# Optimization experiments

Hardware: AMD Instinct MI355X
Metric: run time of the kernel (lower is better)

Reference implementation:

```python
import jax, jax.numpy as jnp
import numpy as np

B, S, E, H = 2, 2048, 2048, 16
D = E // H  # head_dim = 128


def _rope_tables(seq_len, dim):
    # standard RoPE: theta_i = 10000^(-2i/dim), angles duplicated over pair halves
    inv_freq = 1.0 / (10000.0 ** (np.arange(0, dim, 2, dtype=np.float32) / dim))
    angles = np.arange(seq_len, dtype=np.float32)[:, None] * inv_freq[None, :]  # [S, D/2]
    angles = np.concatenate([angles, angles], axis=-1)  # [S, D]
    return jnp.asarray(np.cos(angles)), jnp.asarray(np.sin(angles))


def setup_inputs() -> dict:
    key = jax.random.key(0)
    ks = jax.random.split(key, 10)
    sc = 1.0 / np.sqrt(E)
    cos, sin = _rope_tables(S, D)
    mask = jnp.tril(jnp.ones((S, S), dtype=bool))[None, None]  # causal [1,1,S,S]
    return {
        "x_q": jax.random.normal(ks[0], (B, S, E), jnp.float32),
        "x_kv": jax.random.normal(ks[1], (B, S, E), jnp.float32),
        "cos": cos,
        "sin": sin,
        "wq": jax.random.normal(ks[2], (E, E), jnp.float32) * sc,
        "bq": jax.random.normal(ks[3], (E,), jnp.float32) * 0.01,
        "wk": jax.random.normal(ks[4], (E, E), jnp.float32) * sc,
        "bk": jax.random.normal(ks[5], (E,), jnp.float32) * 0.01,
        "wv": jax.random.normal(ks[6], (E, E), jnp.float32) * sc,
        "bv": jax.random.normal(ks[7], (E,), jnp.float32) * 0.01,
        "wo": jax.random.normal(ks[8], (E, E), jnp.float32) * sc,
        "bo": jax.random.normal(ks[9], (E,), jnp.float32) * 0.01,
        "mask": mask,
    }


def _apply_rope(x, cos, sin):
    # x: [B,H,S,D]; cos/sin: [S,D]. rotate-half convention.
    x1, x2 = jnp.split(x, 2, axis=-1)
    rot = jnp.concatenate([-x2, x1], axis=-1)
    return x * cos[None, None] + rot * sin[None, None]


def reference(x_q, x_kv, cos, sin, wq, bq, wk, bk, wv, bv, wo, bo, mask):
    b, sq, _ = x_q.shape
    skv = x_kv.shape[1]
    q = (x_q @ wq.T + bq).reshape(b, sq, H, D).transpose(0, 2, 1, 3)   # [B,H,Sq,D]
    k = (x_kv @ wk.T + bk).reshape(b, skv, H, D).transpose(0, 2, 1, 3)
    v = (x_kv @ wv.T + bv).reshape(b, skv, H, D).transpose(0, 2, 1, 3)
    q = _apply_rope(q, cos, sin)
    k = _apply_rope(k, cos, sin)
    scores = jnp.einsum("bhqd,bhkd->bhqk", q, k) / jnp.sqrt(jnp.float32(D))
    scores = jnp.where(mask, scores, jnp.float32(-1e9))
    w = jax.nn.softmax(scores, axis=-1)  # dropout p=0 -> identity
    out = jnp.einsum("bhqk,bhkd->bhqd", w, v)
    out = out.transpose(0, 2, 1, 3).reshape(b, sq, H * D)
    return out @ wo.T + bo
```

## Files before the change

kernel.cpp:

```cpp
#include <hip/hip_runtime.h>
#include <hip/hip_bf16.h>

#define Bb 2
#define Ss 2048
#define Ee 2048
#define Hh 16
#define Dd 128
#define Mrows (Bb*Ss)

typedef short short8 __attribute__((ext_vector_type(8)));
typedef float f32x4 __attribute__((ext_vector_type(4)));

__device__ __forceinline__ unsigned short bf_rne(float f) {
    unsigned u = __builtin_bit_cast(unsigned, f);
    u += 0x7fffu + ((u >> 16) & 1u);
    return (unsigned short)(u >> 16);
}
__device__ __forceinline__ float bf2f(unsigned short x) {
    unsigned u = ((unsigned)x) << 16;
    return __builtin_bit_cast(float, u);
}
__device__ __forceinline__ void load_lds16(const void* g, void* l) {
    __builtin_amdgcn_global_load_lds(
        (const __attribute__((address_space(1))) unsigned int*)g,
        (__attribute__((address_space(3))) unsigned int*)l, 16, 0, 0);
}

__global__ void cast_all_kernel(const float4* __restrict__ xq, const float4* __restrict__ xkv,
                                const float4* __restrict__ wq, const float4* __restrict__ wk,
                                const float4* __restrict__ wv, const float4* __restrict__ wo,
                                ushort4* __restrict__ out) {
    int i = blockIdx.x * 256 + threadIdx.x;
    const float4* src;
    int rel;
    if (i < 2097152)       { src = xq;  rel = i; }
    else if (i < 4194304)  { src = xkv; rel = i - 2097152; }
    else if (i < 5242880)  { src = wq;  rel = i - 4194304; }
    else if (i < 6291456)  { src = wk;  rel = i - 5242880; }
    else if (i < 7340032)  { src = wv;  rel = i - 6291456; }
    else                   { src = wo;  rel = i - 7340032; }
    float4 v = src[rel];
    ushort4 o;
    o.x = bf_rne(v.x); o.y = bf_rne(v.y); o.z = bf_rne(v.z); o.w = bf_rne(v.w);
    out[i] = o;
}

#define NTK 64

__device__ __forceinline__ void gemm_core_db(
    const short* __restrict__ A, const short* __restrict__ W,
    int m0, int n0, char* lds, f32x4 (&acc)[8][4], int tid)
{
    const int wid  = tid >> 6, lane = tid & 63;
    const int wr   = wid >> 1, wc   = wid & 1;
    const int quad = lane >> 4, l16 = lane & 15;
    const int lr   = lane >> 3, sl  = lane & 7;
    const int g    = sl ^ lr;
    const int grow = 2*(wid*8 + lr) + (g >> 2);
    const int kcol = (g & 3) * 8;
    const int cx16 = ((((l16 & 1) << 2) + quad) ^ ((l16 >> 1) & 7)) << 4;
    const int arow = (l16 >> 1) << 7;

    const short* Ap = A + (size_t)(m0 + grow) * Ee + kcol;
    const short* Wp = W + (size_t)(n0 + grow) * Ee + kcol;

    #pragma unroll
    for (int i = 0; i < 4; ++i)
        load_lds16(Ap + (size_t)i*64*Ee, lds + i*4096 + wid*1024);
    #pragma unroll
    for (int i = 0; i < 2; ++i)
        load_lds16(Wp + (size_t)i*64*Ee, lds + 16384 + i*4096 + wid*1024);
    Ap += 32; Wp += 32;
    asm volatile("s_waitcnt vmcnt(0)\n\ts_barrier" ::: "memory");

    for (int t = 0; t < NTK; ++t) {
        const int bo = (t & 1) ? 24576 : 0;
        if (t + 1 < NTK) {
            const int so = bo ^ 24576;
            #pragma unroll
            for (int i = 0; i < 4; ++i)
                load_lds16(Ap + (size_t)i*64*Ee, lds + so + i*4096 + wid*1024);
            #pragma unroll
            for (int i = 0; i < 2; ++i)
                load_lds16(Wp + (size_t)i*64*Ee, lds + so + 16384 + i*4096 + wid*1024);
            Ap += 32; Wp += 32;
        }
        const char* Ab2 = lds + bo + wr*8192 + arow + cx16;
        const char* Bb2 = lds + bo + 16384 + wc*4096 + arow + cx16;
        short8 bfr[4];
        #pragma unroll
        for (int j = 0; j < 4; ++j) bfr[j] = *(const short8*)(Bb2 + j*1024);
        __builtin_amdgcn_s_setprio(1);
        #pragma unroll
        for (int i = 0; i < 8; ++i) {
            short8 af = *(const short8*)(Ab2 + i*1024);
            #pragma unroll
            for (int j = 0; j < 4; ++j)
                acc[i][j] = __builtin_amdgcn_mfma_f32_16x16x32_bf16(af, bfr[j], acc[i][j], 0, 0, 0);
        }
        __builtin_amdgcn_s_setprio(0);
        asm volatile("s_waitcnt vmcnt(0)\n\ts_barrier" ::: "memory");
    }
}

#define BUFB 24576

__device__ __forceinline__ void gemm_core(
    const short* __restrict__ A, const short* __restrict__ W,
    int m0, int n0, char* lds, f32x4 (&acc)[8][4], int tid)
{
    const int wid  = tid >> 6, lane = tid & 63;
    const int wr   = wid >> 1, wc   = wid & 1;
    const int quad = lane >> 4, l16 = lane & 15;
    const int lr   = lane >> 3, sl  = lane & 7;
    const int g    = sl ^ lr;
    const int grow = 2*(wid*8 + lr) + (g >> 2);
    const int kcol = (g & 3) * 8;
    const int cx16 = ((((l16 & 1) << 2) + quad) ^ ((l16 >> 1) & 7)) << 4;
    const int arow = (l16 >> 1) << 7;

    const short* Ab = A + (size_t)(m0 + grow) * Ee + kcol;
    const short* Wb = W + (size_t)(n0 + grow) * Ee + kcol;

    auto stageTile = [&](int kt, int so) {
        const short* a = Ab + kt * 32;
        const short* w = Wb + kt * 32;
        #pragma unroll
        for (int i = 0; i < 4; ++i)
            load_lds16(a + (size_t)i*64*Ee, lds + so + i*4096 + wid*1024);
        #pragma unroll
        for (int i = 0; i < 2; ++i)
            load_lds16(w + (size_t)i*64*Ee, lds + so + 16384 + i*4096 + wid*1024);
    };

    stageTile(0, 0);
    stageTile(1, BUFB);
    asm volatile("s_waitcnt vmcnt(6)\n\ts_barrier" ::: "memory");

    int bo = 0, so = 2*BUFB;
    for (int t = 0; t < NTK; ++t) {
        if (t + 2 < NTK) stageTile(t + 2, so);

        const char* Abase = lds + bo + wr*8192 + arow + cx16;
        const char* Bbase = lds + bo + 16384 + wc*4096 + arow + cx16;
        short8 af[8], bfr[4];
        #pragma unroll
        for (int i = 0; i < 8; ++i) af[i] = *(const short8*)(Abase + i*1024);
        #pragma unroll
        for (int j = 0; j < 4; ++j) bfr[j] = *(const short8*)(Bbase + j*1024);

        __builtin_amdgcn_s_setprio(1);
        #pragma unroll
        for (int i = 0; i < 8; ++i)
            #pragma unroll
            for (int j = 0; j < 4; ++j)
                acc[i][j] = __builtin_amdgcn_mfma_f32_16x16x32_bf16(af[i], bfr[j], acc[i][j], 0, 0, 0);
        __builtin_amdgcn_s_setprio(0);

        if (t == NTK - 1) break;
        if (t < NTK - 2) asm volatile("s_waitcnt vmcnt(6)\n\ts_barrier" ::: "memory");
        else             asm volatile("s_waitcnt vmcnt(0)\n\ts_barrier" ::: "memory");
        bo = (bo == 2*BUFB) ? 0 : bo + BUFB;
        so = (so == 2*BUFB) ? 0 : so + BUFB;
    }
}

__global__ __launch_bounds__(256, 3) void qkv_gemm(
    const short* __restrict__ xq, const short* __restrict__ xkv,
    const short* __restrict__ wq, const short* __restrict__ wk, const short* __restrict__ wv,
    const float* __restrict__ bq, const float* __restrict__ bk, const float* __restrict__ bv,
    short* __restrict__ Qr, short* __restrict__ Kr, short* __restrict__ VT)
{
    __shared__ __align__(16) char lds[49152];
    const int tid  = threadIdx.x;
    const int wid  = tid >> 6, lane = tid & 63;
    const int quad = lane >> 4, l16 = lane & 15;
    const int wr   = wid >> 1, wc   = wid & 1;
    const int m0   = blockIdx.x * 256;
    const int sub  = blockIdx.y >> 4;
    const int nb   = blockIdx.y & 15;
    const int n0   = nb * 128;

    const short* A = (sub == 0) ? xq : xkv;
    const short* W = (sub == 0) ? wq : (sub == 1) ? wk : wv;
    const float* bias = (sub == 0) ? bq : (sub == 1) ? bk : bv;

    f32x4 acc[8][4] = {};
    gemm_core_db(A, W, m0, n0, lds, acc, tid);

    const int b0 = m0 >> 11;
    const int s0 = m0 & (Ss - 1);

    if (sub < 2) {
        short* out = sub ? Kr : Qr;
        #pragma unroll
        for (int i = 0; i < 8; ++i)
            #pragma unroll
            for (int j = 0; j < 4; ++j)
                #pragma unroll
                for (int r = 0; r < 4; ++r) {
                    int gm = m0 + wr*128 + i*16 + quad*4 + r;
                    int d  = wc*64 + j*16 + l16;
                    float v = acc[i][j][r] + bias[n0 + d];
                    int b = gm >> 11, s = gm & (Ss - 1);
                    out[(((size_t)(b*Hh + nb)) * Ss + s) * Dd + d] = (short)bf_rne(v);
                }
    } else {
        __syncthreads();
        short* T = (short*)lds + wid * 4608;
        #pragma unroll
        for (int h = 0; h < 2; ++h) {
            #pragma unroll
            for (int i2 = 0; i2 < 4; ++i2) {
                #pragma unroll
                for (int j = 0; j < 4; ++j)
                    #pragma unroll
                    for (int r = 0; r < 4; ++r) {
                        int dl  = j*16 + l16;
                        int slc = i2*16 + quad*4 + r;
                        T[dl*72 + slc] = (short)bf_rne(acc[h*4 + i2][j][r] + bias[n0 + wc*64 + dl]);
                    }
            }
            #pragma unroll
            for (int ss = 0; ss < 8; ++ss) {
                short8 v = *(const short8*)&T[lane*72 + ss*8];
                int dg = wc*64 + lane;
                int sg = s0 + wr*128 + h*64 + ss*8;
                *(short8*)&VT[(((size_t)(b0*Hh + nb)) * Dd + dg) * Ss + sg] = v;
            }
        }
    }
}

__global__ __launch_bounds__(256, 2) void oproj_gemm(
    const short* __restrict__ A, const short* __restrict__ W,
    const float* __restrict__ bias, float* __restrict__ Cf)
{
    __shared__ __align__(16) char lds[73728];
    const int tid  = threadIdx.x;
    const int wid  = tid >> 6, lane = tid & 63;
    const int quad = lane >> 4, l16 = lane & 15;
    const int wr   = wid >> 1, wc   = wid & 1;
    const int m0 = blockIdx.x * 256;
    const int n0 = blockIdx.y * 128;

    f32x4 acc[8][4] = {};
    gemm_core(A, W, m0, n0, lds, acc, tid);

    #pragma unroll
    for (int i = 0; i < 8; ++i)
        #pragma unroll
        for (int j = 0; j < 4; ++j)
            #pragma unroll
            for (int r = 0; r < 4; ++r) {
                int gm = m0 + wr*128 + i*16 + quad*4 + r;
                int gn = n0 + wc*64 + j*16 + l16;
                Cf[(size_t)gm * Ee + gn] = acc[i][j][r] + bias[gn];
            }
}

__global__ void rope_kernel(short* __restrict__ Qr, short* __restrict__ Kr,
                            const float* __restrict__ cosT, const float* __restrict__ sinT) {
    short* X    = blockIdx.y ? Kr : Qr;
    float scale = blockIdx.y ? 1.0f : 0.08838834764831845f;
    int idx = blockIdx.x * 256 + threadIdx.x;
    int d  = idx & 63;
    int s  = (idx >> 6) & (Ss - 1);
    int bh = idx >> 17;
    size_t base = ((size_t)bh * Ss + s) * Dd;
    float x1 = bf2f((unsigned short)X[base + d]);
    float x2 = bf2f((unsigned short)X[base + d + 64]);
    float c  = cosT[s*Dd + d];
    float sn = sinT[s*Dd + d];
    X[base + d]      = (short)bf_rne((x1 * c - x2 * sn) * scale);
    X[base + d + 64] = (short)bf_rne((x2 * c + x1 * sn) * scale);
}

__global__ __launch_bounds__(256, 2) void attn_kernel(
    const short* __restrict__ Q, const short* __restrict__ Kk,
    const short* __restrict__ VT, short* __restrict__ O)
{
    __shared__ short Ks[64*128];
    __shared__ short Vt[2][128*64];
    __shared__ short Pw[4][32*72];

    const int tid  = threadIdx.x;
    const int wave = tid >> 6;
    const int lane = tid & 63;
    const int quad = lane >> 4;
    const int l16  = lane & 15;
    const int mmap = (blockIdx.x + blockIdx.y) & 15;
    const int qt   = (blockIdx.y & 16) ? (15 - mmap) : mmap;
    const int bh = blockIdx.y;
    const int b  = bh >> 4, h = bh & 15;
    const size_t head_off = (size_t)bh * Ss * Dd;
    const short* Kg  = Kk + head_off;
    const short* VTg = VT + head_off;

    auto stageK = [&](int kt) {
        #pragma unroll
        for (int j = 0; j < 4; ++j) {
            int r = wave*16 + j*4 + (lane >> 4);
            int c = (lane & 15) ^ (r & 15);
            load_lds16(Kg + (size_t)(kt*64 + r)*Dd + c*8, &Ks[(wave*16 + j*4)*128]);
        }
    };
    auto stageV = [&](int kt, int buf) {
        #pragma unroll
        for (int j = 0; j < 4; ++j) {
            int r = wave*32 + j*8 + (lane >> 3);
            int c = (lane & 7) ^ (r & 7);
            load_lds16(VTg + (size_t)r*Ss + kt*64 + c*8, &Vt[buf][(wave*32 + j*8)*64]);
        }
    };

    const int qbase = qt*128 + wave*32;
    short8 qf[2][4];
    #pragma unroll
    for (int mi = 0; mi < 2; ++mi)
        #pragma unroll
        for (int ds = 0; ds < 4; ++ds)
            qf[mi][ds] = *(const short8*)&Q[head_off + (size_t)(qbase + mi*16 + l16)*Dd + ds*32 + quad*8];

    f32x4 o[2][8] = {};
    float m_i[2][4], l_i[2][4];
    #pragma unroll
    for (int mi = 0; mi < 2; ++mi)
        #pragma unroll
        for (int r = 0; r < 4; ++r) { m_i[mi][r] = -__builtin_inff(); l_i[mi][r] = 0.f; }

    const int ktiles = 2*qt + 2;
    stageK(0);
    stageV(0, 0);

    for (int kt = 0; kt < ktiles; ++kt) {
        asm volatile("s_waitcnt vmcnt(0)\n\ts_barrier" ::: "memory");
        if (kt + 1 < ktiles) stageV(kt+1, (kt+1)&1);

        f32x4 sc[2][4] = {};
        #pragma unroll
        for (int jk = 0; jk < 4; ++jk)
            #pragma unroll
            for (int ds = 0; ds < 4; ++ds) {
                short8 kf = *(const short8*)&Ks[(jk*16 + l16)*128 + (((ds*4 + quad) ^ l16) * 8)];
                #pragma unroll
                for (int mi = 0; mi < 2; ++mi)
                    sc[mi][jk] = __builtin_amdgcn_mfma_f32_16x16x32_bf16(qf[mi][ds], kf, sc[mi][jk], 0, 0, 0);
            }

        asm volatile("s_waitcnt lgkmcnt(0)\n\ts_barrier" ::: "memory");
        if (kt + 1 < ktiles) stageK(kt+1);

        const int k0 = kt*64;
        #pragma unroll
        for (int mi = 0; mi < 2; ++mi) {
            if (k0 + 63 > qbase + mi*16) {
                #pragma unroll
                for (int jk = 0; jk < 4; ++jk) {
                    int kg = k0 + jk*16 + l16;
                    #pragma unroll
                    for (int r = 0; r < 4; ++r)
                        if (kg > qbase + mi*16 + quad*4 + r) sc[mi][jk][r] = -__builtin_inff();
                }
            }
        }

        float alpha[2][4];
        #pragma unroll
        for (int mi = 0; mi < 2; ++mi)
            #pragma unroll
            for (int r = 0; r < 4; ++r) {
                float mx = fmaxf(fmaxf(sc[mi][0][r], sc[mi][1][r]), fmaxf(sc[mi][2][r], sc[mi][3][r]));
                #pragma unroll
                for (int off = 1; off < 16; off <<= 1)
                    mx = fmaxf(mx, __shfl_xor(mx, off));
                float mn = fmaxf(m_i[mi][r], mx);
                alpha[mi][r] = __expf(m_i[mi][r] - mn);
                m_i[mi][r] = mn;
                float s = 0.f;
                #pragma unroll
                for (int jk = 0; jk < 4; ++jk) {
                    float p = __expf(sc[mi][jk][r] - mn);
                    sc[mi][jk][r] = p;
                    s += p;
                }
                l_i[mi][r] = l_i[mi][r] * alpha[mi][r] + s;
            }

        #pragma unroll
        for (int mi = 0; mi < 2; ++mi)
            #pragma unroll
            for (int jk = 0; jk < 4; ++jk)
                #pragma unroll
                for (int r = 0; r < 4; ++r)
                    Pw[wave][(mi*16 + quad*4 + r)*72 + jk*16 + l16] = (short)bf_rne(sc[mi][jk][r]);

        #pragma unroll
        for (int mi = 0; mi < 2; ++mi)
            #pragma unroll
            for (int dt = 0; dt < 8; ++dt)
                #pragma unroll
                for (int r = 0; r < 4; ++r)
                    o[mi][dt][r] *= alpha[mi][r];

        short8 pa[2][2];
        #pragma unroll
        for (int mi = 0; mi < 2; ++mi)
            #pragma unroll
            for (int kk = 0; kk < 2; ++kk)
                pa[mi][kk] = *(const short8*)&Pw[wave][(mi*16 + l16)*72 + kk*32 + quad*8];

        const short* vb = Vt[kt & 1];
        #pragma unroll
        for (int dt = 0; dt < 8; ++dt)
            #pragma unroll
            for (int kk = 0; kk < 2; ++kk) {
                short8 vf = *(const short8*)&vb[(dt*16 + l16)*64 + (((kk*4 + quad) ^ (l16 & 7)) * 8)];
                #pragma unroll
                for (int mi = 0; mi < 2; ++mi)
                    o[mi][dt] = __builtin_amdgcn_mfma_f32_16x16x32_bf16(pa[mi][kk], vf, o[mi][dt], 0, 0, 0);
            }
    }

    #pragma unroll
    for (int mi = 0; mi < 2; ++mi)
        #pragma unroll
        for (int r = 0; r < 4; ++r) {
            float l = l_i[mi][r];
            #pragma unroll
            for (int off = 1; off < 16; off <<= 1)
                l += __shfl_xor(l, off);
            float inv = 1.0f / l;
            int srow = qbase + mi*16 + quad*4 + r;
            size_t obase = ((size_t)b * Ss + srow) * Ee + h * Dd;
            #pragma unroll
            for (int dt = 0; dt < 8; ++dt)
                O[obase + dt*16 + l16] = (short)bf_rne(o[mi][dt][r] * inv);
        }
}

extern "C" void kernel_launch(void* const* d_in, const int* in_sizes, int n_in,
                              void* d_out, int out_size, void* d_ws, size_t ws_size,
                              hipStream_t stream) {
    const float* x_q  = (const float*)d_in[0];
    const float* x_kv = (const float*)d_in[1];
    const float* cosT = (const float*)d_in[2];
    const float* sinT = (const float*)d_in[3];
    const float* wq = (const float*)d_in[4];
    const float* bq = (const float*)d_in[5];
    const float* wk = (const float*)d_in[6];
    const float* bk = (const float*)d_in[7];
    const float* wv = (const float*)d_in[8];
    const float* bv = (const float*)d_in[9];
    const float* wo = (const float*)d_in[10];
    const float* bo = (const float*)d_in[11];

    size_t off = 0;
    auto alloc = [&](size_t bytes) {
        void* p = (char*)d_ws + off;
        off += (bytes + 255) & ~(size_t)255;
        return p;
    };
    const size_t nX = (size_t)Mrows * Ee;
    const size_t nW = (size_t)Ee * Ee;
    short* xq16  = (short*)alloc(nX * 2);
    short* xkv16 = (short*)alloc(nX * 2);
    short* wq16  = (short*)alloc(nW * 2);
    short* wk16  = (short*)alloc(nW * 2);
    short* wv16  = (short*)alloc(nW * 2);
    short* wo16  = (short*)alloc(nW * 2);
    short* Qr    = (short*)alloc(nX * 2);
    short* Kr    = (short*)alloc(nX * 2);
    short* VTb   = (short*)alloc(nX * 2);
    short* Ob    = (short*)alloc(nX * 2);

    cast_all_kernel<<<32768, 256, 0, stream>>>(
        (const float4*)x_q, (const float4*)x_kv, (const float4*)wq,
        (const float4*)wk, (const float4*)wv, (const float4*)wo, (ushort4*)xq16);

    qkv_gemm<<<dim3(Mrows/256, 48), 256, 0, stream>>>(
        xq16, xkv16, wq16, wk16, wv16, bq, bk, bv, Qr, Kr, VTb);

    rope_kernel<<<dim3((Bb*Hh*Ss*64)/256, 2), 256, 0, stream>>>(Qr, Kr, cosT, sinT);

    attn_kernel<<<dim3(16, Bb*Hh), 256, 0, stream>>>(Qr, Kr, VTb, Ob);

    oproj_gemm<<<dim3(Mrows/256, Ee/128), 256, 0, stream>>>(Ob, wo16, bo, (float*)d_out);
}
```

Measured before the change: 437.3 us.

## Fuse RoPE and Q scaling into QKV GEMM epilogue via per-wave full-head tiles

Changes the QKV GEMM wave tiling so that each wave owns 64 rows by all 128 head columns instead of a 128x64 quadrant. Each thread then holds both halves of every rotate-half pair, so RoPE and the Q scaling can be applied in the epilogue. The separate rope kernel, with its extra read and write pass over Q and K, is removed. The cost is that each wave now loads all 8 B fragments per k-step instead of 4, and the epilogue now reads cos/sin tables.

```diff
diff --git a/kernel.cpp b/kernel.cpp
--- a/kernel.cpp
+++ b/kernel.cpp
@@ -47,12 +47,11 @@
 
 #define NTK 64
 
-__device__ __forceinline__ void gemm_core_db(
+__device__ __forceinline__ void gemm_core_qkv(
     const short* __restrict__ A, const short* __restrict__ W,
-    int m0, int n0, char* lds, f32x4 (&acc)[8][4], int tid)
+    int m0, int n0, char* lds, f32x4 (&acc)[4][8], int tid)
 {
     const int wid  = tid >> 6, lane = tid & 63;
-    const int wr   = wid >> 1, wc   = wid & 1;
     const int quad = lane >> 4, l16 = lane & 15;
     const int lr   = lane >> 3, sl  = lane & 7;
     const int g    = sl ^ lr;
@@ -85,18 +84,18 @@
                 load_lds16(Wp + (size_t)i*64*Ee, lds + so + 16384 + i*4096 + wid*1024);
             Ap += 32; Wp += 32;
         }
-        const char* Ab2 = lds + bo + wr*8192 + arow + cx16;
-        const char* Bb2 = lds + bo + 16384 + wc*4096 + arow + cx16;
-        short8 bfr[4];
-        #pragma unroll
-        for (int j = 0; j < 4; ++j) bfr[j] = *(const short8*)(Bb2 + j*1024);
+        const char* Ab2 = lds + bo + wid*4096 + arow + cx16;
+        const char* Bb2 = lds + bo + 16384 + arow + cx16;
+        short8 af[4];
+        #pragma unroll
+        for (int i = 0; i < 4; ++i) af[i] = *(const short8*)(Ab2 + i*1024);
         __builtin_amdgcn_s_setprio(1);
         #pragma unroll
-        for (int i = 0; i < 8; ++i) {
-            short8 af = *(const short8*)(Ab2 + i*1024);
-            #pragma unroll
-            for (int j = 0; j < 4; ++j)
-                acc[i][j] = __builtin_amdgcn_mfma_f32_16x16x32_bf16(af, bfr[j], acc[i][j], 0, 0, 0);
+        for (int j = 0; j < 8; ++j) {
+            short8 bfr = *(const short8*)(Bb2 + j*1024);
+            #pragma unroll
+            for (int i = 0; i < 4; ++i)
+                acc[i][j] = __builtin_amdgcn_mfma_f32_16x16x32_bf16(af[i], bfr, acc[i][j], 0, 0, 0);
         }
         __builtin_amdgcn_s_setprio(0);
         asm volatile("s_waitcnt vmcnt(0)\n\ts_barrier" ::: "memory");
@@ -169,13 +168,13 @@
     const short* __restrict__ xq, const short* __restrict__ xkv,
     const short* __restrict__ wq, const short* __restrict__ wk, const short* __restrict__ wv,
     const float* __restrict__ bq, const float* __restrict__ bk, const float* __restrict__ bv,
+    const float* __restrict__ cosT, const float* __restrict__ sinT,
     short* __restrict__ Qr, short* __restrict__ Kr, short* __restrict__ VT)
 {
     __shared__ __align__(16) char lds[49152];
     const int tid  = threadIdx.x;
     const int wid  = tid >> 6, lane = tid & 63;
     const int quad = lane >> 4, l16 = lane & 15;
-    const int wr   = wid >> 1, wc   = wid & 1;
     const int m0   = blockIdx.x * 256;
     const int sub  = blockIdx.y >> 4;
     const int nb   = blockIdx.y & 15;
@@ -185,47 +184,53 @@
     const short* W = (sub == 0) ? wq : (sub == 1) ? wk : wv;
     const float* bias = (sub == 0) ? bq : (sub == 1) ? bk : bv;
 
-    f32x4 acc[8][4] = {};
-    gemm_core_db(A, W, m0, n0, lds, acc, tid);
+    f32x4 acc[4][8] = {};
+    gemm_core_qkv(A, W, m0, n0, lds, acc, tid);
 
     const int b0 = m0 >> 11;
     const int s0 = m0 & (Ss - 1);
 
     if (sub < 2) {
         short* out = sub ? Kr : Qr;
-        #pragma unroll
-        for (int i = 0; i < 8; ++i)
-            #pragma unroll
-            for (int j = 0; j < 4; ++j)
-                #pragma unroll
-                for (int r = 0; r < 4; ++r) {
-                    int gm = m0 + wr*128 + i*16 + quad*4 + r;
-                    int d  = wc*64 + j*16 + l16;
-                    float v = acc[i][j][r] + bias[n0 + d];
-                    int b = gm >> 11, s = gm & (Ss - 1);
-                    out[(((size_t)(b*Hh + nb)) * Ss + s) * Dd + d] = (short)bf_rne(v);
+        const float scale = sub ? 1.0f : 0.08838834764831845f;
+        #pragma unroll
+        for (int i = 0; i < 4; ++i)
+            #pragma unroll
+            for (int r = 0; r < 4; ++r) {
+                int gm = m0 + wid*64 + i*16 + quad*4 + r;
+                int b = gm >> 11, s = gm & (Ss - 1);
+                size_t rowbase = (((size_t)(b*Hh + nb)) * Ss + s) * Dd;
+                #pragma unroll
+                for (int j = 0; j < 4; ++j) {
+                    int d = j*16 + l16;
+                    float c  = cosT[s*Dd + d];
+                    float sn = sinT[s*Dd + d];
+                    float x1 = acc[i][j][r]     + bias[n0 + d];
+                    float x2 = acc[i][j + 4][r] + bias[n0 + d + 64];
+                    out[rowbase + d]      = (short)bf_rne((x1 * c - x2 * sn) * scale);
+                    out[rowbase + d + 64] = (short)bf_rne((x2 * c + x1 * sn) * scale);
                 }
+            }
     } else {
         __syncthreads();
         short* T = (short*)lds + wid * 4608;
         #pragma unroll
-        for (int h = 0; h < 2; ++h) {
-            #pragma unroll
-            for (int i2 = 0; i2 < 4; ++i2) {
+        for (int h2 = 0; h2 < 2; ++h2) {
+            #pragma unroll
+            for (int i = 0; i < 4; ++i)
                 #pragma unroll
                 for (int j = 0; j < 4; ++j)
                     #pragma unroll
                     for (int r = 0; r < 4; ++r) {
                         int dl  = j*16 + l16;
-                        int slc = i2*16 + quad*4 + r;
-                        T[dl*72 + slc] = (short)bf_rne(acc[h*4 + i2][j][r] + bias[n0 + wc*64 + dl]);
+                        int slc = i*16 + quad*4 + r;
+                        T[dl*72 + slc] = (short)bf_rne(acc[i][h2*4 + j][r] + bias[n0 + h2*64 + dl]);
                     }
-            }
             #pragma unroll
             for (int ss = 0; ss < 8; ++ss) {
                 short8 v = *(const short8*)&T[lane*72 + ss*8];
-                int dg = wc*64 + lane;
-                int sg = s0 + wr*128 + h*64 + ss*8;
+                int dg = h2*64 + lane;
+                int sg = s0 + wid*64 + ss*8;
                 *(short8*)&VT[(((size_t)(b0*Hh + nb)) * Dd + dg) * Ss + sg] = v;
             }
         }
@@ -257,23 +262,6 @@
                 int gn = n0 + wc*64 + j*16 + l16;
                 Cf[(size_t)gm * Ee + gn] = acc[i][j][r] + bias[gn];
             }
-}
-
-__global__ void rope_kernel(short* __restrict__ Qr, short* __restrict__ Kr,
-                            const float* __restrict__ cosT, const float* __restrict__ sinT) {
-    short* X    = blockIdx.y ? Kr : Qr;
-    float scale = blockIdx.y ? 1.0f : 0.08838834764831845f;
-    int idx = blockIdx.x * 256 + threadIdx.x;
-    int d  = idx & 63;
-    int s  = (idx >> 6) & (Ss - 1);
-    int bh = idx >> 17;
-    size_t base = ((size_t)bh * Ss + s) * Dd;
-    float x1 = bf2f((unsigned short)X[base + d]);
-    float x2 = bf2f((unsigned short)X[base + d + 64]);
-    float c  = cosT[s*Dd + d];
-    float sn = sinT[s*Dd + d];
-    X[base + d]      = (short)bf_rne((x1 * c - x2 * sn) * scale);
-    X[base + d + 64] = (short)bf_rne((x2 * c + x1 * sn) * scale);
 }
 
 __global__ __launch_bounds__(256, 2) void attn_kernel(
@@ -479,9 +467,7 @@
         (const float4*)wk, (const float4*)wv, (const float4*)wo, (ushort4*)xq16);
 
     qkv_gemm<<<dim3(Mrows/256, 48), 256, 0, stream>>>(
-        xq16, xkv16, wq16, wk16, wv16, bq, bk, bv, Qr, Kr, VTb);
-
-    rope_kernel<<<dim3((Bb*Hh*Ss*64)/256, 2), 256, 0, stream>>>(Qr, Kr, cosT, sinT);
+        xq16, xkv16, wq16, wk16, wv16, bq, bk, bv, cosT, sinT, Qr, Kr, VTb);
 
     attn_kernel<<<dim3(16, Bb*Hh), 256, 0, stream>>>(Qr, Kr, VTb, Ob);
 
```

After: 436.0 us. Within noise of the previous version (-0.3%).
